# Kernel optimization log

Hardware: AMD Instinct MI355X
Metric: run time of the kernel (lower is better)

The kernel has to match this reference:

```python
import jax, jax.numpy as jnp
import numpy as np

GROUPS = 32
EPS = 1e-5


def group_norm(x, gamma, beta):
    # x: [B,H,W,C], channels_last, groups over channel dim (Keras GroupNormalization default)
    B, H, W, C = x.shape
    xg = x.reshape(B, H, W, GROUPS, C // GROUPS)
    mean = xg.mean(axis=(1, 2, 4), keepdims=True)
    var = xg.var(axis=(1, 2, 4), keepdims=True)
    xn = ((xg - mean) * jax.lax.rsqrt(var + EPS)).reshape(B, H, W, C)
    return xn * gamma + beta


def conv1x1(x, w, b):
    # 1x1 conv == per-pixel dense: [B,H,W,C] x [C,D] -> [B,H,W,D]
    return jnp.einsum('bhwc,cd->bhwd', x, w) + b


def setup_inputs() -> dict:
    key = jax.random.key(0)
    ks = jax.random.split(key, 10)
    C = 512
    s = 1.0 / np.sqrt(C)
    inp = {
        'x': jax.random.normal(ks[0], (2, 64, 64, C), dtype=jnp.float32),
        'gamma': jnp.ones((C,), jnp.float32),
        'beta': jnp.zeros((C,), jnp.float32),
        'wq': jax.random.normal(ks[1], (C, C), jnp.float32) * s,
        'bq': jnp.zeros((C,), jnp.float32),
        'wk': jax.random.normal(ks[2], (C, C), jnp.float32) * s,
        'bk': jnp.zeros((C,), jnp.float32),
        'wv': jax.random.normal(ks[3], (C, C), jnp.float32) * s,
        'bv': jnp.zeros((C,), jnp.float32),
        'wp': jax.random.normal(ks[4], (C, C), jnp.float32) * s,
        'bp': jnp.zeros((C,), jnp.float32),
    }
    return inp


def reference(x, gamma, beta, wq, bq, wk, bk, wv, bv, wp, bp):
    B, H, W, C = x.shape
    N = H * W
    xn = group_norm(x, gamma, beta)
    q = conv1x1(xn, wq, bq).reshape(B, N, C)
    k = conv1x1(xn, wk, bk).reshape(B, N, C)
    v = conv1x1(xn, wv, bv).reshape(B, N, C)
    scale = 1.0 / jnp.sqrt(jnp.asarray(C, x.dtype))
    scores = jnp.einsum('bnc,bmc->bnm', q, k) * scale  # [B,N,N]
    attn = jax.nn.softmax(scores, axis=-1)
    out = jnp.einsum('bnm,bmc->bnc', attn, v).reshape(B, H, W, C)
    return conv1x1(out, wp, bp) + x
```

## Files before the change

kernel.cpp:

```cpp
#include <hip/hip_runtime.h>
#include <hip/hip_fp16.h>

typedef _Float16 half_t;
typedef _Float16 half8 __attribute__((ext_vector_type(8)));
typedef float floatx4 __attribute__((ext_vector_type(4)));

static constexpr int BATCH = 2;
static constexpr int NSP = 4096;
static constexpr int CH = 512;
static constexpr int NQKV = 3 * CH;
static constexpr int KSPLIT = 4;

static constexpr size_t OFF_STATS = 0;
static constexpr size_t OFF_ROWSUM = 512;
static constexpr size_t OFF_PST = 33280;
static constexpr size_t OFF_WQKV = 196608;
static constexpr size_t WQKV_BYTES = (size_t)NQKV * CH * 2;
static constexpr size_t OFF_WP = OFF_WQKV + WQKV_BYTES;
static constexpr size_t WP_BYTES = (size_t)CH * CH * 2;
static constexpr size_t OFF_XN = OFF_WP + WP_BYTES;
static constexpr size_t XN_BYTES = (size_t)BATCH * NSP * CH * 2;
static constexpr size_t OFF_QKV = OFF_XN + XN_BYTES;
static constexpr size_t QKV_BYTES = (size_t)BATCH * NSP * NQKV * 2;
static constexpr size_t OFF_VT = OFF_QKV + QKV_BYTES;
static constexpr size_t OFF_AO = OFF_VT + XN_BYTES;
static constexpr size_t OFF_S = OFF_AO + XN_BYTES;
static constexpr size_t S_BYTES_1 = (size_t)NSP * NSP * 2;
static constexpr size_t OFF_PART = OFF_XN;

__device__ __forceinline__ void gld16(void* lds, const void* g) {
  __builtin_amdgcn_global_load_lds(
      (__attribute__((address_space(1))) void*)(g),
      (__attribute__((address_space(3))) void*)(lds),
      16, 0, 0);
}

__global__ __launch_bounds__(256) void gn_stats(const float* __restrict__ x,
                                                float* __restrict__ pst) {
  int b = blockIdx.y;
  int tid = (int)threadIdx.x;
  int g = ((tid * 4) & (CH - 1)) >> 4;
  const float* base = x + (long)b * NSP * CH + (long)blockIdx.x * 16 * CH + tid * 4;
  float s = 0.f, s2 = 0.f;
#pragma unroll
  for (int it = 0; it < 8; ++it) {
    floatx4 v = *(const floatx4*)(base + (long)it * 1024);
#pragma unroll
    for (int r = 0; r < 4; ++r) { s += v[r]; s2 += v[r] * v[r]; }
  }
  __shared__ float gs[32], gs2[32];
  if (tid < 32) { gs[tid] = 0.f; gs2[tid] = 0.f; }
  __syncthreads();
  atomicAdd(&gs[g], s);
  atomicAdd(&gs2[g], s2);
  __syncthreads();
  if (tid < 32) {
    long idx = ((long)(b * 256 + blockIdx.x) * 32 + tid) * 2;
    pst[idx] = gs[tid];
    pst[idx + 1] = gs2[tid];
  }
}

__global__ __launch_bounds__(256) void gn_finalize(const float* __restrict__ pst,
                                                   float* __restrict__ st,
                                                   float* __restrict__ rowsum) {
  int tid = (int)threadIdx.x;
  int bg = tid & 63;
  int p = tid >> 6;
  int b = bg >> 5, g = bg & 31;
  float s = 0.f, s2 = 0.f;
  for (int j = 0; j < 64; ++j) {
    int chunk = p * 64 + j;
    long idx = ((long)(b * 256 + chunk) * 32 + g) * 2;
    s += pst[idx];
    s2 += pst[idx + 1];
  }
  __shared__ float rs[64][4], rs2[64][4];
  rs[bg][p] = s;
  rs2[bg][p] = s2;
  __syncthreads();
  if (tid < 64) {
    float ts = rs[tid][0] + rs[tid][1] + rs[tid][2] + rs[tid][3];
    float ts2 = rs2[tid][0] + rs2[tid][1] + rs2[tid][2] + rs2[tid][3];
    const float inv = 1.f / 65536.f;
    float mean = ts * inv;
    float var = ts2 * inv - mean * mean;
    st[tid * 2] = mean;
    st[tid * 2 + 1] = rsqrtf(var + 1e-5f);
  }
  floatx4* rz = (floatx4*)rowsum;
#pragma unroll
  for (int j = 0; j < 8; ++j)
    rz[tid + j * 256] = floatx4{0.f, 0.f, 0.f, 0.f};
}

__global__ __launch_bounds__(256) void gn_apply(const float* __restrict__ x,
                                                const float* __restrict__ st,
                                                const float* __restrict__ gamma,
                                                const float* __restrict__ beta,
                                                half_t* __restrict__ xn) {
  long i = ((long)blockIdx.x * 256 + threadIdx.x) * 8;
  int c = (int)(i & (CH - 1));
  int b = (int)(i >> 21);
  int g = c >> 4;
  float mean = st[((b << 5) + g) * 2];
  float rstd = st[((b << 5) + g) * 2 + 1];
  floatx4 a = *(const floatx4*)(x + i);
  floatx4 d = *(const floatx4*)(x + i + 4);
  half8 o;
#pragma unroll
  for (int r = 0; r < 4; ++r) {
    o[r]     = (half_t)((a[r] - mean) * rstd * gamma[c + r] + beta[c + r]);
    o[r + 4] = (half_t)((d[r] - mean) * rstd * gamma[c + r + 4] + beta[c + r + 4]);
  }
  *(half8*)(xn + i) = o;
}

__global__ __launch_bounds__(256) void transpose_w(
    const float* __restrict__ w0, const float* __restrict__ w1,
    const float* __restrict__ w2, const float* __restrict__ w3,
    half_t* __restrict__ o0, half_t* __restrict__ o1,
    half_t* __restrict__ o2, half_t* __restrict__ o3) {
  const float* w; half_t* o;
  switch (blockIdx.z) {
    case 0: w = w0; o = o0; break;
    case 1: w = w1; o = o1; break;
    case 2: w = w2; o = o2; break;
    default: w = w3; o = o3; break;
  }
  __shared__ float t[32][33];
  int d0 = blockIdx.x * 32, c0 = blockIdx.y * 32;
  int tx = threadIdx.x & 31, ty = threadIdx.x >> 5;
#pragma unroll
  for (int i = 0; i < 4; ++i)
    t[ty + i * 8][tx] = w[(long)(c0 + ty + i * 8) * CH + d0 + tx];
  __syncthreads();
#pragma unroll
  for (int i = 0; i < 4; ++i) {
    int d = ty + i * 8;
    o[(long)(d0 + d) * CH + c0 + tx] = (half_t)t[tx][d];
  }
}

__global__ __launch_bounds__(256) void transpose_v(const half_t* __restrict__ v,
                                                   half_t* __restrict__ vt) {
  __shared__ half_t t[32][33];
  int b = blockIdx.z;
  int d0 = blockIdx.x * 32, n0 = blockIdx.y * 32;
  int tx = threadIdx.x & 31, ty = threadIdx.x >> 5;
  const half_t* vb = v + (long)b * NSP * NQKV;
  half_t* ob = vt + (long)b * NSP * CH;
#pragma unroll
  for (int i = 0; i < 4; ++i)
    t[ty + i * 8][tx] = vb[(long)(n0 + ty + i * 8) * NQKV + d0 + tx];
  __syncthreads();
#pragma unroll
  for (int i = 0; i < 4; ++i) {
    int d = ty + i * 8;
    ob[(long)(d0 + d) * NSP + n0 + tx] = t[tx][d];
  }
}

template <int BM, int BN, int BK, int EPI, int SWZ, int KSP, typename OutT>
__global__ __launch_bounds__(256) void gemm_nt(
    const half_t* __restrict__ X, const half_t* __restrict__ Y,
    OutT* __restrict__ Co, const float* __restrict__ b0,
    const float* __restrict__ b1, const float* __restrict__ b2,
    const float* __restrict__ resid, float* __restrict__ rowsum,
    int M, int N, int K, int ldx, int ldy, int ldc,
    long xbs, long ybs, long cbs, float scale) {
  constexpr int SM = BM / 32;
  constexpr int SN = BN / 32;
  constexpr int ROWS = BM + BN;
  constexpr int CPR = BK / 8;
  constexpr int RPW = 64 / CPR;
  constexpr int ROUNDS = (ROWS * BK * 2) / 4096;
  constexpr int KSTEPS = BK / 32;
  static_assert(BM % (4 * RPW) == 0, "no As/Bs straddle within a round");
  __shared__ __align__(16) half_t Sh[ROWS * BK];

  const int zb = blockIdx.z / KSP;
  const int ks = blockIdx.z % KSP;
  int bx, by;
  if (SWZ == 1) {
    int lin = (int)(blockIdx.x + gridDim.x * blockIdx.y);
    int wmt = 256 / (int)gridDim.x;
    by = wmt * (lin >> 8) + ((lin & 255) % wmt);
    bx = (lin & 255) / wmt;
  } else if (SWZ == 2) {
    by = blockIdx.x;
    bx = blockIdx.y;
  } else {
    bx = blockIdx.x;
    by = blockIdx.y;
  }

  const half_t* Xb = X + (long)zb * xbs + (long)ks * K;
  const half_t* Yb = Y + (long)zb * ybs + (long)ks * K;
  OutT* Cb = Co + (long)blockIdx.z * cbs;

  const int m0 = by * BM;
  const int n0 = bx * BN;
  const int tid = (int)threadIdx.x;
  const int wave = tid >> 6;
  const int lane = tid & 63;
  const int quad = lane >> 4;
  const int l16 = lane & 15;
  const int wm = wave >> 1;
  const int wn = wave & 1;

  floatx4 acc[SM][SN] = {};

  const int srow = lane / CPR;
  const int schunk = lane % CPR;
  const char* Xc = (const char*)Xb;

  int soff[ROUNDS];
#pragma unroll
  for (int r = 0; r < ROUNDS; ++r) {
    int row = r * (4 * RPW) + wave * RPW + srow;
    int gchunk = schunk ^ (row & (CPR - 1));
    const char* p = (row < BM)
        ? (const char*)(Xb + (long)(m0 + row) * ldx)
        : (const char*)(Yb + (long)(n0 + row - BM) * ldy);
    soff[r] = (int)(p + gchunk * 16 - Xc);
  }

  int offA[SM], offB[SN];
#pragma unroll
  for (int i = 0; i < SM; ++i) {
    int m = wm * (BM / 2) + i * 16 + l16;
    int cc = quad ^ (m & (CPR - 1));
    offA[i] = (m * BK + cc * 8) * 2;
  }
#pragma unroll
  for (int j = 0; j < SN; ++j) {
    int n = wn * (BN / 2) + j * 16 + l16;
    int cc = quad ^ (n & (CPR - 1));
    offB[j] = (BM * BK + n * BK + cc * 8) * 2;
  }

  for (int k0 = 0; k0 < K; k0 += BK) {
#pragma unroll
    for (int r = 0; r < ROUNDS; ++r) {
      gld16((char*)Sh + (r * 4 + wave) * 1024, Xc + (long)soff[r]);
      soff[r] += BK * 2;
    }
    __syncthreads();

#pragma unroll
    for (int kk = 0; kk < KSTEPS; ++kk) {
      const int kx = kk << 6;
      half8 af[SM], bf[SN];
#pragma unroll
      for (int i = 0; i < SM; ++i)
        af[i] = *(const half8*)((const char*)Sh + (offA[i] ^ kx));
#pragma unroll
      for (int j = 0; j < SN; ++j)
        bf[j] = *(const half8*)((const char*)Sh + (offB[j] ^ kx));
#pragma unroll
      for (int i = 0; i < SM; ++i)
#pragma unroll
        for (int j = 0; j < SN; ++j)
          acc[i][j] = __builtin_amdgcn_mfma_f32_16x16x32_f16(af[i], bf[j], acc[i][j], 0, 0, 0);
    }
    __syncthreads();
  }

#pragma unroll
  for (int i = 0; i < SM; ++i) {
    int gmb = m0 + wm * (BM / 2) + i * 16 + quad * 4;
    float rs[4] = {0.f, 0.f, 0.f, 0.f};
#pragma unroll
    for (int j = 0; j < SN; ++j) {
      int gn = n0 + wn * (BN / 2) + j * 16 + l16;
      float bias = 0.f, sc = 1.f;
      if (EPI == 1) {
        if (gn < CH) { bias = b0[gn]; sc = scale; }
        else if (gn < 2 * CH) { bias = b1[gn - CH]; }
        else { bias = b2[gn - 2 * CH]; }
      } else if (EPI == 2) {
        bias = b0[gn];
      }
#pragma unroll
      for (int r = 0; r < 4; ++r) {
        long idx = (long)(gmb + r) * ldc + gn;
        float v = acc[i][j][r];
        if (EPI == 1) v = (v + bias) * sc;
        if (EPI == 2) v = v + bias + resid[idx];
        if (EPI == 3) { v = __expf(v); rs[r] += v; }
        Cb[idx] = (OutT)v;
      }
    }
    if (EPI == 3) {
#pragma unroll
      for (int r = 0; r < 4; ++r) {
        float v = rs[r];
        v += __shfl_xor(v, 1);
        v += __shfl_xor(v, 2);
        v += __shfl_xor(v, 4);
        v += __shfl_xor(v, 8);
        if (l16 == 0) atomicAdd(&rowsum[(long)zb * NSP + gmb + r], v);
      }
    }
  }
}

__global__ __launch_bounds__(256) void pv_combine(const half_t* __restrict__ part,
                                                  const float* __restrict__ rowsum,
                                                  half_t* __restrict__ ao) {
  const long bNC = (long)NSP * CH;
  long i = ((long)blockIdx.x * 256 + threadIdx.x) * 8;
  int b = (int)(i >> 21);
  long inner = i & ((1L << 21) - 1);
  float inv = 1.f / rowsum[i >> 9];
  float s[8] = {};
#pragma unroll
  for (int ks = 0; ks < KSPLIT; ++ks) {
    half8 h = *(const half8*)(part + ((long)(b * KSPLIT + ks)) * bNC + inner);
#pragma unroll
    for (int r = 0; r < 8; ++r) s[r] += (float)h[r];
  }
  half8 o;
#pragma unroll
  for (int r = 0; r < 8; ++r) o[r] = (half_t)(s[r] * inv);
  *(half8*)(ao + i) = o;
}

extern "C" void kernel_launch(void* const* d_in, const int* in_sizes, int n_in,
                              void* d_out, int out_size, void* d_ws, size_t ws_size,
                              hipStream_t stream) {
  const float* x = (const float*)d_in[0];
  const float* gamma = (const float*)d_in[1];
  const float* beta = (const float*)d_in[2];
  const float* wq = (const float*)d_in[3];
  const float* bq = (const float*)d_in[4];
  const float* wk = (const float*)d_in[5];
  const float* bk = (const float*)d_in[6];
  const float* wv = (const float*)d_in[7];
  const float* bv = (const float*)d_in[8];
  const float* wp = (const float*)d_in[9];
  const float* bp = (const float*)d_in[10];
  float* out = (float*)d_out;
  char* ws = (char*)d_ws;

  float* st = (float*)(ws + OFF_STATS);
  float* rsum = (float*)(ws + OFF_ROWSUM);
  float* pst = (float*)(ws + OFF_PST);
  half_t* wqkvT = (half_t*)(ws + OFF_WQKV);
  half_t* wpT = (half_t*)(ws + OFF_WP);
  half_t* xn = (half_t*)(ws + OFF_XN);
  half_t* qkv = (half_t*)(ws + OFF_QKV);
  half_t* vt = (half_t*)(ws + OFF_VT);
  half_t* ao = (half_t*)(ws + OFF_AO);
  half_t* S = (half_t*)(ws + OFF_S);
  half_t* part = (half_t*)(ws + OFF_PART);

  half_t* q = qkv;
  half_t* k = qkv + CH;
  half_t* v = qkv + 2 * CH;

  const float scale = 0.044194173824159216f;
  const long bQKV = (long)NSP * NQKV;
  const long bNC = (long)NSP * CH;
  const long bNN = (long)NSP * NSP;

  gn_stats<<<dim3(256, BATCH), 256, 0, stream>>>(x, pst);
  gn_finalize<<<1, 256, 0, stream>>>(pst, st, rsum);
  gn_apply<<<2048, 256, 0, stream>>>(x, st, gamma, beta, xn);
  transpose_w<<<dim3(16, 16, 4), 256, 0, stream>>>(
      wq, wk, wv, wp, wqkvT, wqkvT + (size_t)CH * CH, wqkvT + 2 * (size_t)CH * CH, wpT);

  gemm_nt<128, 128, 64, 1, 2, 1, half_t><<<dim3(BATCH * NSP / 128, NQKV / 128, 1), 256, 0, stream>>>(
      xn, wqkvT, qkv, bq, bk, bv, nullptr, nullptr, BATCH * NSP, NQKV, CH,
      CH, CH, NQKV, 0, 0, 0, scale);
  transpose_v<<<dim3(16, 128, BATCH), 256, 0, stream>>>(v, vt);

  bool full = ws_size >= OFF_S + 2 * S_BYTES_1;
  if (full) {
    gemm_nt<128, 128, 64, 3, 1, 1, half_t><<<dim3(32, 32, BATCH), 256, 0, stream>>>(
        q, k, S, nullptr, nullptr, nullptr, nullptr, rsum, NSP, NSP, CH,
        NQKV, NQKV, NSP, bQKV, bQKV, bNN, 1.f);
    gemm_nt<128, 128, 64, 0, 2, KSPLIT, half_t><<<dim3(NSP / 128, CH / 128, BATCH * KSPLIT), 256, 0, stream>>>(
        S, vt, part, nullptr, nullptr, nullptr, nullptr, nullptr, NSP, CH, NSP / KSPLIT,
        NSP, NSP, CH, bNN, bNC, bNC, 1.f);
    pv_combine<<<2048, 256, 0, stream>>>(part, rsum, ao);
  } else {
    for (int bb = 0; bb < BATCH; ++bb) {
      gemm_nt<128, 128, 64, 3, 1, 1, half_t><<<dim3(32, 32, 1), 256, 0, stream>>>(
          q + bb * bQKV, k + bb * bQKV, S, nullptr, nullptr, nullptr, nullptr,
          rsum + bb * NSP, NSP, NSP, CH, NQKV, NQKV, NSP, 0, 0, 0, 1.f);
      gemm_nt<128, 128, 64, 0, 2, KSPLIT, half_t><<<dim3(NSP / 128, CH / 128, KSPLIT), 256, 0, stream>>>(
          S, vt + bb * bNC, part + (long)bb * KSPLIT * bNC, nullptr, nullptr, nullptr,
          nullptr, nullptr, NSP, CH, NSP / KSPLIT, NSP, NSP, CH, 0, 0, bNC, 1.f);
    }
    pv_combine<<<2048, 256, 0, stream>>>(part, rsum, ao);
  }
  gemm_nt<64, 64, 128, 2, 2, 1, float><<<dim3(BATCH * NSP / 64, CH / 64, 1), 256, 0, stream>>>(
      ao, wpT, out, bp, nullptr, nullptr, x, nullptr, BATCH * NSP, CH, CH,
      CH, CH, CH, 0, 0, 0, 1.f);
}
```

Baseline: 262.7 us.

## Fold group-norm into per-batch QKV weights and fuse V transpose into GEMM epilogue

Group-norm scaling (rstd*gamma, plus the q softmax scale) is folded into per-batch copies of the QKV weights, and the mean/beta shift is folded into a per-batch bias computed by a new bias_prep kernel. The QKV GEMM can then consume a plain fp16 cast of x, which the stats kernel writes while it reduces, so gn_apply goes away. The V slice is transposed through LDS in the QKV GEMM epilogue and written straight to vt, so the separate transpose_v kernel goes away. In exchange the kernel adds a serial-loop bias kernel, keeps two weight copies, and quantises x to fp16 before normalisation, which risks precision loss when the group mean is large.

```diff
diff --git a/kernel.cpp b/kernel.cpp
--- a/kernel.cpp
+++ b/kernel.cpp
@@ -2,6 +2,7 @@
 #include <hip/hip_fp16.h>
 
 typedef _Float16 half_t;
+typedef _Float16 half4 __attribute__((ext_vector_type(4)));
 typedef _Float16 half8 __attribute__((ext_vector_type(8)));
 typedef float floatx4 __attribute__((ext_vector_type(4)));
 
@@ -10,23 +11,23 @@
 static constexpr int CH = 512;
 static constexpr int NQKV = 3 * CH;
 static constexpr int KSPLIT = 4;
+static constexpr float QSCALE = 0.044194173824159216f;
 
 static constexpr size_t OFF_STATS = 0;
 static constexpr size_t OFF_ROWSUM = 512;
-static constexpr size_t OFF_PST = 33280;
-static constexpr size_t OFF_WQKV = 196608;
-static constexpr size_t WQKV_BYTES = (size_t)NQKV * CH * 2;
-static constexpr size_t OFF_WP = OFF_WQKV + WQKV_BYTES;
-static constexpr size_t WP_BYTES = (size_t)CH * CH * 2;
-static constexpr size_t OFF_XN = OFF_WP + WP_BYTES;
+static constexpr size_t OFF_B2 = 33280;
+static constexpr size_t OFF_PST = 45568;
+static constexpr size_t OFF_W2 = 196608;
+static constexpr size_t OFF_WP = OFF_W2 + (size_t)2 * NQKV * CH * 2;
+static constexpr size_t OFF_X16 = OFF_WP + (size_t)CH * CH * 2;
 static constexpr size_t XN_BYTES = (size_t)BATCH * NSP * CH * 2;
-static constexpr size_t OFF_QKV = OFF_XN + XN_BYTES;
+static constexpr size_t OFF_QKV = OFF_X16 + XN_BYTES;
 static constexpr size_t QKV_BYTES = (size_t)BATCH * NSP * NQKV * 2;
 static constexpr size_t OFF_VT = OFF_QKV + QKV_BYTES;
 static constexpr size_t OFF_AO = OFF_VT + XN_BYTES;
 static constexpr size_t OFF_S = OFF_AO + XN_BYTES;
 static constexpr size_t S_BYTES_1 = (size_t)NSP * NSP * 2;
-static constexpr size_t OFF_PART = OFF_XN;
+static constexpr size_t OFF_PART = OFF_X16;
 
 __device__ __forceinline__ void gld16(void* lds, const void* g) {
   __builtin_amdgcn_global_load_lds(
@@ -35,18 +36,28 @@
       16, 0, 0);
 }
 
-__global__ __launch_bounds__(256) void gn_stats(const float* __restrict__ x,
-                                                float* __restrict__ pst) {
+__global__ __launch_bounds__(256) void gn_cast_stats(const float* __restrict__ x,
+                                                     half_t* __restrict__ x16,
+                                                     float* __restrict__ pst) {
   int b = blockIdx.y;
   int tid = (int)threadIdx.x;
-  int g = ((tid * 4) & (CH - 1)) >> 4;
-  const float* base = x + (long)b * NSP * CH + (long)blockIdx.x * 16 * CH + tid * 4;
+  int g = ((tid * 8) & (CH - 1)) >> 4;
+  long base = (long)b * NSP * CH + (long)blockIdx.x * 16 * CH + tid * 8;
   float s = 0.f, s2 = 0.f;
 #pragma unroll
-  for (int it = 0; it < 8; ++it) {
-    floatx4 v = *(const floatx4*)(base + (long)it * 1024);
-#pragma unroll
-    for (int r = 0; r < 4; ++r) { s += v[r]; s2 += v[r] * v[r]; }
+  for (int it = 0; it < 4; ++it) {
+    long idx = base + (long)it * 2048;
+    floatx4 a = *(const floatx4*)(x + idx);
+    floatx4 d = *(const floatx4*)(x + idx + 4);
+    half8 o;
+#pragma unroll
+    for (int r = 0; r < 4; ++r) {
+      s += a[r] + d[r];
+      s2 += a[r] * a[r] + d[r] * d[r];
+      o[r] = (half_t)a[r];
+      o[r + 4] = (half_t)d[r];
+    }
+    *(half8*)(x16 + idx) = o;
   }
   __shared__ float gs[32], gs2[32];
   if (tid < 32) { gs[tid] = 0.f; gs2[tid] = 0.f; }
@@ -94,39 +105,18 @@
     rz[tid + j * 256] = floatx4{0.f, 0.f, 0.f, 0.f};
 }
 
-__global__ __launch_bounds__(256) void gn_apply(const float* __restrict__ x,
-                                                const float* __restrict__ st,
-                                                const float* __restrict__ gamma,
-                                                const float* __restrict__ beta,
-                                                half_t* __restrict__ xn) {
-  long i = ((long)blockIdx.x * 256 + threadIdx.x) * 8;
-  int c = (int)(i & (CH - 1));
-  int b = (int)(i >> 21);
-  int g = c >> 4;
-  float mean = st[((b << 5) + g) * 2];
-  float rstd = st[((b << 5) + g) * 2 + 1];
-  floatx4 a = *(const floatx4*)(x + i);
-  floatx4 d = *(const floatx4*)(x + i + 4);
-  half8 o;
-#pragma unroll
-  for (int r = 0; r < 4; ++r) {
-    o[r]     = (half_t)((a[r] - mean) * rstd * gamma[c + r] + beta[c + r]);
-    o[r + 4] = (half_t)((d[r] - mean) * rstd * gamma[c + r + 4] + beta[c + r + 4]);
-  }
-  *(half8*)(xn + i) = o;
-}
-
 __global__ __launch_bounds__(256) void transpose_w(
     const float* __restrict__ w0, const float* __restrict__ w1,
     const float* __restrict__ w2, const float* __restrict__ w3,
-    half_t* __restrict__ o0, half_t* __restrict__ o1,
-    half_t* __restrict__ o2, half_t* __restrict__ o3) {
-  const float* w; half_t* o;
-  switch (blockIdx.z) {
-    case 0: w = w0; o = o0; break;
-    case 1: w = w1; o = o1; break;
-    case 2: w = w2; o = o2; break;
-    default: w = w3; o = o3; break;
+    half_t* __restrict__ wqkv2, half_t* __restrict__ wpT,
+    const float* __restrict__ st, const float* __restrict__ gamma) {
+  int z = blockIdx.z;
+  const float* w;
+  switch (z) {
+    case 0: w = w0; break;
+    case 1: w = w1; break;
+    case 2: w = w2; break;
+    default: w = w3; break;
   }
   __shared__ float t[32][33];
   int d0 = blockIdx.x * 32, c0 = blockIdx.y * 32;
@@ -135,40 +125,60 @@
   for (int i = 0; i < 4; ++i)
     t[ty + i * 8][tx] = w[(long)(c0 + ty + i * 8) * CH + d0 + tx];
   __syncthreads();
-#pragma unroll
-  for (int i = 0; i < 4; ++i) {
-    int d = ty + i * 8;
-    o[(long)(d0 + d) * CH + c0 + tx] = (half_t)t[tx][d];
-  }
-}
-
-__global__ __launch_bounds__(256) void transpose_v(const half_t* __restrict__ v,
-                                                   half_t* __restrict__ vt) {
-  __shared__ half_t t[32][33];
-  int b = blockIdx.z;
-  int d0 = blockIdx.x * 32, n0 = blockIdx.y * 32;
-  int tx = threadIdx.x & 31, ty = threadIdx.x >> 5;
-  const half_t* vb = v + (long)b * NSP * NQKV;
-  half_t* ob = vt + (long)b * NSP * CH;
-#pragma unroll
-  for (int i = 0; i < 4; ++i)
-    t[ty + i * 8][tx] = vb[(long)(n0 + ty + i * 8) * NQKV + d0 + tx];
-  __syncthreads();
-#pragma unroll
-  for (int i = 0; i < 4; ++i) {
-    int d = ty + i * 8;
-    ob[(long)(d0 + d) * NSP + n0 + tx] = t[tx][d];
-  }
+  if (z == 3) {
+#pragma unroll
+    for (int i = 0; i < 4; ++i) {
+      int d = ty + i * 8;
+      wpT[(long)(d0 + d) * CH + c0 + tx] = (half_t)t[tx][d];
+    }
+  } else {
+    int c = c0 + tx, g = c >> 4;
+    float qs = (z == 0) ? QSCALE : 1.f;
+#pragma unroll
+    for (int b = 0; b < BATCH; ++b) {
+      float sfac = st[((b << 5) + g) * 2 + 1] * gamma[c] * qs;
+#pragma unroll
+      for (int i = 0; i < 4; ++i) {
+        int d = ty + i * 8;
+        wqkv2[(long)b * NQKV * CH + (long)(z * CH + d0 + d) * CH + c] =
+            (half_t)(t[tx][d] * sfac);
+      }
+    }
+  }
+}
+
+__global__ __launch_bounds__(256) void bias_prep(
+    const float* __restrict__ wq, const float* __restrict__ wk,
+    const float* __restrict__ wv, const float* __restrict__ bq,
+    const float* __restrict__ bk, const float* __restrict__ bv,
+    const float* __restrict__ st, const float* __restrict__ gamma,
+    const float* __restrict__ beta, float* __restrict__ b2) {
+  int d = blockIdx.x * 256 + (int)threadIdx.x;
+  int b = blockIdx.y;
+  int wi = d >> 9, dd = d & 511;
+  const float* w = wi == 0 ? wq : (wi == 1 ? wk : wv);
+  const float* bias = wi == 0 ? bq : (wi == 1 ? bk : bv);
+  float acc = 0.f;
+  for (int c = 0; c < CH; ++c) {
+    int g = c >> 4;
+    float mean = st[((b << 5) + g) * 2];
+    float rstd = st[((b << 5) + g) * 2 + 1];
+    float coef = beta[c] - mean * rstd * gamma[c];
+    acc += coef * w[(long)c * CH + dd];
+  }
+  float r = bias[dd] + acc;
+  if (wi == 0) r *= QSCALE;
+  b2[b * NQKV + d] = r;
 }
 
 template <int BM, int BN, int BK, int EPI, int SWZ, int KSP, typename OutT>
 __global__ __launch_bounds__(256) void gemm_nt(
     const half_t* __restrict__ X, const half_t* __restrict__ Y,
     OutT* __restrict__ Co, const float* __restrict__ b0,
-    const float* __restrict__ b1, const float* __restrict__ b2,
     const float* __restrict__ resid, float* __restrict__ rowsum,
+    half_t* __restrict__ aux,
     int M, int N, int K, int ldx, int ldy, int ldc,
-    long xbs, long ybs, long cbs, float scale) {
+    long xbs, long ybs, long cbs) {
   constexpr int SM = BM / 32;
   constexpr int SN = BN / 32;
   constexpr int ROWS = BM + BN;
@@ -176,8 +186,9 @@
   constexpr int RPW = 64 / CPR;
   constexpr int ROUNDS = (ROWS * BK * 2) / 4096;
   constexpr int KSTEPS = BK / 32;
+  constexpr int LDSH = (EPI == 1 && ROWS * BK < 17408) ? 17408 : ROWS * BK;
   static_assert(BM % (4 * RPW) == 0, "no As/Bs straddle within a round");
-  __shared__ __align__(16) half_t Sh[ROWS * BK];
+  __shared__ __align__(16) half_t Sh[LDSH];
 
   const int zb = blockIdx.z / KSP;
   const int ks = blockIdx.z % KSP;
@@ -267,6 +278,33 @@
     __syncthreads();
   }
 
+  if (EPI == 1 && n0 >= 2 * CH) {
+    constexpr int TP = 136;
+#pragma unroll
+    for (int i = 0; i < SM; ++i) {
+      int mb = wm * (BM / 2) + i * 16 + quad * 4;
+#pragma unroll
+      for (int j = 0; j < SN; ++j) {
+        int dl = wn * (BN / 2) + j * 16 + l16;
+        float bias = b0[zb * NQKV + n0 + dl];
+        half4 h;
+#pragma unroll
+        for (int r = 0; r < 4; ++r) h[r] = (half_t)(acc[i][j][r] + bias);
+        *(half4*)(Sh + dl * TP + mb) = h;
+      }
+    }
+    __syncthreads();
+    int tx = tid & 15, ty = tid >> 4;
+    half_t* vtb = aux + (long)zb * NSP * CH;
+#pragma unroll
+    for (int jj = 0; jj < 8; ++jj) {
+      int d = ty + jj * 16;
+      half8 h = *(const half8*)(Sh + d * TP + tx * 8);
+      *(half8*)(vtb + (long)(n0 - 2 * CH + d) * NSP + m0 + tx * 8) = h;
+    }
+    return;
+  }
+
 #pragma unroll
   for (int i = 0; i < SM; ++i) {
     int gmb = m0 + wm * (BM / 2) + i * 16 + quad * 4;
@@ -274,19 +312,14 @@
 #pragma unroll
     for (int j = 0; j < SN; ++j) {
       int gn = n0 + wn * (BN / 2) + j * 16 + l16;
-      float bias = 0.f, sc = 1.f;
-      if (EPI == 1) {
-        if (gn < CH) { bias = b0[gn]; sc = scale; }
-        else if (gn < 2 * CH) { bias = b1[gn - CH]; }
-        else { bias = b2[gn - 2 * CH]; }
-      } else if (EPI == 2) {
-        bias = b0[gn];
-      }
+      float bias = 0.f;
+      if (EPI == 1) bias = b0[zb * NQKV + gn];
+      else if (EPI == 2) bias = b0[gn];
 #pragma unroll
       for (int r = 0; r < 4; ++r) {
         long idx = (long)(gmb + r) * ldc + gn;
         float v = acc[i][j][r];
-        if (EPI == 1) v = (v + bias) * sc;
+        if (EPI == 1) v += bias;
         if (EPI == 2) v = v + bias + resid[idx];
         if (EPI == 3) { v = __expf(v); rs[r] += v; }
         Cb[idx] = (OutT)v;
@@ -346,10 +379,11 @@
 
   float* st = (float*)(ws + OFF_STATS);
   float* rsum = (float*)(ws + OFF_ROWSUM);
+  float* b2 = (float*)(ws + OFF_B2);
   float* pst = (float*)(ws + OFF_PST);
-  half_t* wqkvT = (half_t*)(ws + OFF_WQKV);
+  half_t* w2 = (half_t*)(ws + OFF_W2);
   half_t* wpT = (half_t*)(ws + OFF_WP);
-  half_t* xn = (half_t*)(ws + OFF_XN);
+  half_t* x16 = (half_t*)(ws + OFF_X16);
   half_t* qkv = (half_t*)(ws + OFF_QKV);
   half_t* vt = (half_t*)(ws + OFF_VT);
   half_t* ao = (half_t*)(ws + OFF_AO);
@@ -358,45 +392,41 @@
 
   half_t* q = qkv;
   half_t* k = qkv + CH;
-  half_t* v = qkv + 2 * CH;
-
-  const float scale = 0.044194173824159216f;
+
   const long bQKV = (long)NSP * NQKV;
   const long bNC = (long)NSP * CH;
   const long bNN = (long)NSP * NSP;
 
-  gn_stats<<<dim3(256, BATCH), 256, 0, stream>>>(x, pst);
+  gn_cast_stats<<<dim3(256, BATCH), 256, 0, stream>>>(x, x16, pst);
   gn_finalize<<<1, 256, 0, stream>>>(pst, st, rsum);
-  gn_apply<<<2048, 256, 0, stream>>>(x, st, gamma, beta, xn);
-  transpose_w<<<dim3(16, 16, 4), 256, 0, stream>>>(
-      wq, wk, wv, wp, wqkvT, wqkvT + (size_t)CH * CH, wqkvT + 2 * (size_t)CH * CH, wpT);
-
-  gemm_nt<128, 128, 64, 1, 2, 1, half_t><<<dim3(BATCH * NSP / 128, NQKV / 128, 1), 256, 0, stream>>>(
-      xn, wqkvT, qkv, bq, bk, bv, nullptr, nullptr, BATCH * NSP, NQKV, CH,
-      CH, CH, NQKV, 0, 0, 0, scale);
-  transpose_v<<<dim3(16, 128, BATCH), 256, 0, stream>>>(v, vt);
+  transpose_w<<<dim3(16, 16, 4), 256, 0, stream>>>(wq, wk, wv, wp, w2, wpT, st, gamma);
+  bias_prep<<<dim3(6, BATCH), 256, 0, stream>>>(wq, wk, wv, bq, bk, bv, st, gamma, beta, b2);
+
+  gemm_nt<128, 128, 64, 1, 2, 1, half_t><<<dim3(NSP / 128, NQKV / 128, BATCH), 256, 0, stream>>>(
+      x16, w2, qkv, b2, nullptr, nullptr, vt, NSP, NQKV, CH,
+      CH, CH, NQKV, bNC, (long)NQKV * CH, bQKV);
 
   bool full = ws_size >= OFF_S + 2 * S_BYTES_1;
   if (full) {
     gemm_nt<128, 128, 64, 3, 1, 1, half_t><<<dim3(32, 32, BATCH), 256, 0, stream>>>(
-        q, k, S, nullptr, nullptr, nullptr, nullptr, rsum, NSP, NSP, CH,
-        NQKV, NQKV, NSP, bQKV, bQKV, bNN, 1.f);
+        q, k, S, nullptr, nullptr, rsum, nullptr, NSP, NSP, CH,
+        NQKV, NQKV, NSP, bQKV, bQKV, bNN);
     gemm_nt<128, 128, 64, 0, 2, KSPLIT, half_t><<<dim3(NSP / 128, CH / 128, BATCH * KSPLIT), 256, 0, stream>>>(
-        S, vt, part, nullptr, nullptr, nullptr, nullptr, nullptr, NSP, CH, NSP / KSPLIT,
-        NSP, NSP, CH, bNN, bNC, bNC, 1.f);
+        S, vt, part, nullptr, nullptr, nullptr, nullptr, NSP, CH, NSP / KSPLIT,
+        NSP, NSP, CH, bNN, bNC, bNC);
     pv_combine<<<2048, 256, 0, stream>>>(part, rsum, ao);
   } else {
     for (int bb = 0; bb < BATCH; ++bb) {
       gemm_nt<128, 128, 64, 3, 1, 1, half_t><<<dim3(32, 32, 1), 256, 0, stream>>>(
-          q + bb * bQKV, k + bb * bQKV, S, nullptr, nullptr, nullptr, nullptr,
-          rsum + bb * NSP, NSP, NSP, CH, NQKV, NQKV, NSP, 0, 0, 0, 1.f);
+          q + bb * bQKV, k + bb * bQKV, S, nullptr, nullptr, rsum + bb * NSP, nullptr,
+          NSP, NSP, CH, NQKV, NQKV, NSP, 0, 0, 0);
       gemm_nt<128, 128, 64, 0, 2, KSPLIT, half_t><<<dim3(NSP / 128, CH / 128, KSPLIT), 256, 0, stream>>>(
           S, vt + bb * bNC, part + (long)bb * KSPLIT * bNC, nullptr, nullptr, nullptr,
-          nullptr, nullptr, NSP, CH, NSP / KSPLIT, NSP, NSP, CH, 0, 0, bNC, 1.f);
+          nullptr, NSP, CH, NSP / KSPLIT, NSP, NSP, CH, 0, 0, bNC);
     }
     pv_combine<<<2048, 256, 0, stream>>>(part, rsum, ao);
   }
   gemm_nt<64, 64, 128, 2, 2, 1, float><<<dim3(BATCH * NSP / 64, CH / 64, 1), 256, 0, stream>>>(
-      ao, wpT, out, bp, nullptr, nullptr, x, nullptr, BATCH * NSP, CH, CH,
-      CH, CH, CH, 0, 0, 0, 1.f);
-}
+      ao, wpT, out, bp, x, nullptr, nullptr, BATCH * NSP, CH, CH,
+      CH, CH, CH, 0, 0, 0);
+}
```

Result: slower. 280.6 us (+6.8%).
